# Optimization experiments

Hardware: AMD Instinct MI355X
Metric: run time of the kernel (lower is better)

The kernel has to match this reference:

```python
import jax, jax.numpy as jnp
import numpy as np

N, E = 50000, 500000
T, R, H, DK = 3, 5, 8, 16
IN = OUT = 128
SQRT_DK = float(np.sqrt(DK))
LN_EPS = 1e-5


def setup_inputs() -> dict:
    key = jax.random.key(0)
    ks = jax.random.split(key, 20)
    s = 0.05
    return {
        "x": jax.random.normal(ks[0], (N, IN), jnp.float32),
        "node_type": jax.random.randint(ks[1], (N,), 0, T),
        "src": jax.random.randint(ks[2], (E,), 0, N),
        "dst": jax.random.randint(ks[3], (E,), 0, N),
        "etype": jax.random.randint(ks[4], (E,), 0, R),
        "Wk": jax.random.normal(ks[5], (T, IN, OUT), jnp.float32) * s,
        "bk": jnp.zeros((T, OUT), jnp.float32),
        "Wq": jax.random.normal(ks[6], (T, IN, OUT), jnp.float32) * s,
        "bq": jnp.zeros((T, OUT), jnp.float32),
        "Wv": jax.random.normal(ks[7], (T, IN, OUT), jnp.float32) * s,
        "bv": jnp.zeros((T, OUT), jnp.float32),
        "Wa": jax.random.normal(ks[8], (T, OUT, OUT), jnp.float32) * s,
        "ba": jnp.zeros((T, OUT), jnp.float32),
        "rel_pri": jnp.ones((R, H), jnp.float32),
        "rel_att": jax.random.normal(ks[9], (R, H, DK, DK), jnp.float32) * s,
        "rel_msg": jax.random.normal(ks[10], (R, H, DK, DK), jnp.float32) * s,
        "skip": jnp.ones((T,), jnp.float32),
        "ln_g": jnp.ones((T, OUT), jnp.float32),
        "ln_b": jnp.zeros((T, OUT), jnp.float32),
    }


def _typed_proj(x, node_type, W, b):
    # apply all per-ntype Linears, then pick each node's own type
    y = jnp.einsum('ni,tio->nto', x, W) + b[None]            # [N,T,OUT]
    return jnp.take_along_axis(y, node_type[:, None, None], axis=1)[:, 0]


def reference(x, node_type, src, dst, etype, Wk, bk, Wq, bq, Wv, bv, Wa, ba,
              rel_pri, rel_att, rel_msg, skip, ln_g, ln_b):
    n = x.shape[0]
    k = _typed_proj(x, node_type, Wk, bk).reshape(n, H, DK)
    q = _typed_proj(x, node_type, Wq, bq).reshape(n, H, DK)
    v = _typed_proj(x, node_type, Wv, bv).reshape(n, H, DK)

    ks_e, vs_e, q_e = k[src], v[src], q[dst]                 # [E,H,DK]
    # relation-specific bmm: loop over the small fixed set of etypes
    key_e = jnp.zeros_like(ks_e)
    val_e = jnp.zeros_like(vs_e)
    for r in range(R):
        sel = (etype == r)[:, None, None].astype(x.dtype)
        key_e = key_e + sel * jnp.einsum('ehd,hdf->ehf', ks_e, rel_att[r])
        val_e = val_e + sel * jnp.einsum('ehd,hdf->ehf', vs_e, rel_msg[r])

    a = (q_e * key_e).sum(-1) * rel_pri[etype] / SQRT_DK     # [E,H]

    # segment softmax: per-(dst, etype) mailbox, matching DGL per-etype reduce
    seg = dst * R + etype
    NR = n * R
    m = jax.ops.segment_max(a, seg, num_segments=NR)         # [NR,H]
    m = jnp.where(jnp.isfinite(m), m, 0.0)
    p = jnp.exp(a - m[seg])
    denom = jax.ops.segment_sum(p, seg, num_segments=NR)
    attw = p / denom[seg]                                    # [E,H]

    h_seg = jax.ops.segment_sum(attw[..., None] * val_e, seg,
                                num_segments=NR).reshape(n, R, H, DK)
    cnt = jax.ops.segment_sum(jnp.ones((a.shape[0],), x.dtype), seg,
                              num_segments=NR).reshape(n, R)
    has = (cnt > 0).astype(x.dtype)                          # etypes with messages
    # cross_reducer='mean': average over etypes that delivered messages
    t = (h_seg * has[..., None, None]).sum(1)
    t = t / jnp.maximum(has.sum(1), 1.0)[:, None, None]
    t = t.reshape(n, OUT)

    trans = _typed_proj(t, node_type, Wa, ba)
    alpha = jax.nn.sigmoid(skip)[node_type][:, None]
    out = trans * alpha + x * (1.0 - alpha)

    # per-ntype LayerNorm (dropout is identity in eval)
    mu = out.mean(-1, keepdims=True)
    var = ((out - mu) ** 2).mean(-1, keepdims=True)
    out = (out - mu) * jax.lax.rsqrt(var + LN_EPS)
    out = out * ln_g[node_type] + ln_b[node_type]
    return out
```

## Files before the change

kernel.cpp:

```cpp
#include <hip/hip_runtime.h>
#include <math.h>

#define N_NODES 50000
#define N_EDGES 500000
#define NT 3
#define NRR 5
#define NH 8
#define DKH 16
#define DIM 128
#define NSEG (N_NODES * NRR)

__global__ void init_ints(int* __restrict__ base, long n_ints) {
  long i = (long)blockIdx.x * blockDim.x + threadIdx.x;
  long stride = (long)gridDim.x * blockDim.x;
  for (long j = i; j < n_ints; j += stride) base[j] = 0;
}

__global__ void bucket_nodes(const int* __restrict__ ntype, int* __restrict__ order,
                             int* __restrict__ bcnt) {
  __shared__ int lcnt[NT];
  __shared__ int lbase[NT];
  int tid = threadIdx.x;
  if (tid < NT) lcnt[tid] = 0;
  __syncthreads();
  int i = blockIdx.x * blockDim.x + tid;
  int t = -1, lp = 0;
  if (i < N_NODES) {
    t = ntype[i];
    lp = atomicAdd(&lcnt[t], 1);
  }
  __syncthreads();
  if (tid < NT) lbase[tid] = atomicAdd(&bcnt[tid], lcnt[tid]);
  __syncthreads();
  if (i < N_NODES) order[t * N_NODES + lbase[t] + lp] = i;
}

__global__ void hist_seg(const int* __restrict__ dst, const int* __restrict__ etype,
                         int* __restrict__ deg) {
  int i = blockIdx.x * blockDim.x + threadIdx.x;
  if (i >= N_EDGES) return;
  atomicAdd(&deg[dst[i] * NRR + etype[i]], 1);
}

__global__ void assign_seg(const int* __restrict__ deg, int* __restrict__ segstart,
                           int* __restrict__ gcursor) {
  int i = blockIdx.x * 256 + threadIdx.x;
  int lane = threadIdx.x & 63, wv = threadIdx.x >> 6;
  int d = (i < NSEG) ? deg[i] : 0;
  int s = d;
  #pragma unroll
  for (int m = 1; m < 64; m <<= 1) {
    int v = __shfl_up(s, m, 64);
    if (lane >= m) s += v;
  }
  __shared__ int wsum[4];
  __shared__ int wbase[4];
  __shared__ int blockbase;
  if (lane == 63) wsum[wv] = s;
  __syncthreads();
  if (threadIdx.x == 0) {
    int acc = 0;
    #pragma unroll
    for (int w = 0; w < 4; w++) { wbase[w] = acc; acc += wsum[w]; }
    blockbase = atomicAdd(gcursor, acc);
  }
  __syncthreads();
  if (i < NSEG) segstart[i] = blockbase + wbase[wv] + (s - d);
}

__global__ void scatter_seg(const int* __restrict__ src, const int* __restrict__ dst,
                            const int* __restrict__ etype,
                            const int* __restrict__ segstart, int* __restrict__ cursor,
                            int* __restrict__ meta) {
  int i = blockIdx.x * blockDim.x + threadIdx.x;
  if (i >= N_EDGES) return;
  int seg = dst[i] * NRR + etype[i];
  int pos = segstart[seg] + atomicAdd(&cursor[seg], 1);
  meta[pos] = src[i];
}

template<bool FUSED>
__launch_bounds__(256)
__global__ void typed_gemm(const float* __restrict__ in, const float* __restrict__ W,
                           const float* __restrict__ bias, float* __restrict__ out,
                           const int* __restrict__ order, const int* __restrict__ bcnt,
                           const float* __restrict__ hseg, const float* __restrict__ denom) {
  int t = blockIdx.y;
  int cnt = bcnt[t];
  int base = blockIdx.x * 64;
  if (base >= cnt) return;

  __shared__ float xs[64][129];
  __shared__ __align__(16) float wsl[16 * 128];
  __shared__ int nids[64];

  int tid = threadIdx.x;
  if (tid < 64) {
    int idx = base + tid;
    nids[tid] = (idx < cnt) ? order[t * N_NODES + idx] : -1;
  }
  __syncthreads();

  #pragma unroll
  for (int i = 0; i < 8; i++) {
    int idx = tid + i * 256;
    int node = idx >> 5;
    int c4 = idx & 31;
    int nid = nids[node];
    float4 v = make_float4(0.f, 0.f, 0.f, 0.f);
    if (nid >= 0) {
      if (FUSED) {
        int h = c4 >> 2;
        float cn = 0.f;
        float4 a = make_float4(0.f, 0.f, 0.f, 0.f);
        #pragma unroll
        for (int rr = 0; rr < NRR; rr++) {
          float den = denom[((size_t)nid * NRR + rr) * NH + h];
          if (den > 0.f) {
            float4 hv = *(const float4*)(hseg + ((size_t)nid * NRR + rr) * DIM + c4 * 4);
            a.x += hv.x; a.y += hv.y; a.z += hv.z; a.w += hv.w;
            cn += 1.f;
          }
        }
        float s = 1.f / fmaxf(cn, 1.f);
        v = make_float4(a.x * s, a.y * s, a.z * s, a.w * s);
      } else {
        v = *(const float4*)(in + (size_t)nid * DIM + c4 * 4);
      }
    }
    xs[node][c4 * 4 + 0] = v.x;
    xs[node][c4 * 4 + 1] = v.y;
    xs[node][c4 * 4 + 2] = v.z;
    xs[node][c4 * 4 + 3] = v.w;
  }

  const float* wbase = W + (size_t)t * DIM * DIM;
  int tx = tid & 15;
  int ty = tid >> 4;
  float4 acc[4][2];
  #pragma unroll
  for (int j = 0; j < 4; j++) {
    acc[j][0] = make_float4(0.f, 0.f, 0.f, 0.f);
    acc[j][1] = make_float4(0.f, 0.f, 0.f, 0.f);
  }

  for (int ks = 0; ks < 8; ks++) {
    __syncthreads();
    {
      const float4* g = (const float4*)(wbase + ks * 2048 + tid * 8);
      float4 w0 = g[0], w1 = g[1];
      *(float4*)&wsl[tid * 8] = w0;
      *(float4*)&wsl[tid * 8 + 4] = w1;
    }
    __syncthreads();
    #pragma unroll
    for (int kk = 0; kk < 16; kk++) {
      float4 w0 = *(const float4*)&wsl[kk * 128 + tx * 8];
      float4 w1 = *(const float4*)&wsl[kk * 128 + tx * 8 + 4];
      #pragma unroll
      for (int j = 0; j < 4; j++) {
        float xv = xs[ty * 4 + j][ks * 16 + kk];
        acc[j][0].x += xv * w0.x; acc[j][0].y += xv * w0.y;
        acc[j][0].z += xv * w0.z; acc[j][0].w += xv * w0.w;
        acc[j][1].x += xv * w1.x; acc[j][1].y += xv * w1.y;
        acc[j][1].z += xv * w1.z; acc[j][1].w += xv * w1.w;
      }
    }
  }

  float4 b0 = *(const float4*)(bias + t * DIM + tx * 8);
  float4 b1 = *(const float4*)(bias + t * DIM + tx * 8 + 4);
  #pragma unroll
  for (int j = 0; j < 4; j++) {
    int nid = nids[ty * 4 + j];
    if (nid < 0) continue;
    float4 o0 = make_float4(acc[j][0].x + b0.x, acc[j][0].y + b0.y,
                            acc[j][0].z + b0.z, acc[j][0].w + b0.w);
    float4 o1 = make_float4(acc[j][1].x + b1.x, acc[j][1].y + b1.y,
                            acc[j][1].z + b1.z, acc[j][1].w + b1.w);
    *(float4*)(out + (size_t)nid * DIM + tx * 8) = o0;
    *(float4*)(out + (size_t)nid * DIM + tx * 8 + 4) = o1;
  }
}

__launch_bounds__(256)
__global__ void rel_gather(const float* __restrict__ kmat, const float* __restrict__ qmat,
                           const float* __restrict__ vmat,
                           const float* __restrict__ rel_att, const float* __restrict__ rel_msg,
                           const float* __restrict__ rel_pri,
                           const int* __restrict__ segstart, const int* __restrict__ deg,
                           const int* __restrict__ meta,
                           float* __restrict__ denom, float* __restrict__ hseg) {
  int r = blockIdx.y;
  int tid = threadIdx.x;

  __shared__ __align__(16) float As[8 * 260];
  __shared__ __align__(16) float Ms[8 * 260];
  {
    int idx = tid * 8;
    int hh = idx >> 8, w = idx & 255;
    const float4* ga = (const float4*)(rel_att + (size_t)r * 2048 + idx);
    *(float4*)&As[hh * 260 + w] = ga[0];
    *(float4*)&As[hh * 260 + w + 4] = ga[1];
    const float4* gm = (const float4*)(rel_msg + (size_t)r * 2048 + idx);
    *(float4*)&Ms[hh * 260 + w] = gm[0];
    *(float4*)&Ms[hh * 260 + w + 4] = gm[1];
  }
  __syncthreads();

  int g = tid >> 3;
  int c = tid & 7;
  int n = blockIdx.x * 32 + g;
  if (n >= N_NODES) return;
  int seg = n * NRR + r;
  int dg = deg[seg];
  if (dg == 0) {
    denom[(size_t)seg * NH + c] = 0.f;
    return;
  }
  int p0 = segstart[seg];
  float pri = rel_pri[r * NH + c] * 0.25f;

  const float4* qr = (const float4*)(qmat + (size_t)n * DIM + c * DKH);
  float4 q0 = qr[0], q1 = qr[1], q2 = qr[2], q3 = qr[3];

  float qa[16];
  #pragma unroll
  for (int d = 0; d < 16; d++) {
    const float* ar = &As[c * 260 + d * 16];
    float4 a0 = *(const float4*)(ar);
    float4 a1 = *(const float4*)(ar + 4);
    float4 a2 = *(const float4*)(ar + 8);
    float4 a3 = *(const float4*)(ar + 12);
    qa[d] = a0.x*q0.x + a0.y*q0.y + a0.z*q0.z + a0.w*q0.w
          + a1.x*q1.x + a1.y*q1.y + a1.z*q1.z + a1.w*q1.w
          + a2.x*q2.x + a2.y*q2.y + a2.z*q2.z + a2.w*q2.w
          + a3.x*q3.x + a3.y*q3.y + a3.z*q3.z + a3.w*q3.w;
  }

  float den = 0.f;
  float pv[16];
  #pragma unroll
  for (int d = 0; d < 16; d++) pv[d] = 0.f;

  for (int e = 0; e < dg; e++) {
    int sn = meta[p0 + e];
    const float4* kr = (const float4*)(kmat + (size_t)sn * DIM + c * DKH);
    float4 k0 = kr[0], k1 = kr[1], k2 = kr[2], k3 = kr[3];
    const float4* vr = (const float4*)(vmat + (size_t)sn * DIM + c * DKH);
    float4 v0 = vr[0], v1 = vr[1], v2 = vr[2], v3 = vr[3];
    float s = k0.x*qa[0]  + k0.y*qa[1]  + k0.z*qa[2]  + k0.w*qa[3]
            + k1.x*qa[4]  + k1.y*qa[5]  + k1.z*qa[6]  + k1.w*qa[7]
            + k2.x*qa[8]  + k2.y*qa[9]  + k2.z*qa[10] + k2.w*qa[11]
            + k3.x*qa[12] + k3.y*qa[13] + k3.z*qa[14] + k3.w*qa[15];
    float p = __expf(s * pri);
    den += p;
    pv[0]  += p*v0.x; pv[1]  += p*v0.y; pv[2]  += p*v0.z; pv[3]  += p*v0.w;
    pv[4]  += p*v1.x; pv[5]  += p*v1.y; pv[6]  += p*v1.z; pv[7]  += p*v1.w;
    pv[8]  += p*v2.x; pv[9]  += p*v2.y; pv[10] += p*v2.z; pv[11] += p*v2.w;
    pv[12] += p*v3.x; pv[13] += p*v3.y; pv[14] += p*v3.z; pv[15] += p*v3.w;
  }

  float o[16];
  #pragma unroll
  for (int j = 0; j < 16; j++) o[j] = 0.f;
  #pragma unroll
  for (int d = 0; d < 16; d++) {
    const float* mr = &Ms[c * 260 + d * 16];
    float4 m0 = *(const float4*)(mr);
    float4 m1 = *(const float4*)(mr + 4);
    float4 m2 = *(const float4*)(mr + 8);
    float4 m3 = *(const float4*)(mr + 12);
    float p = pv[d];
    o[0]  += p*m0.x; o[1]  += p*m0.y; o[2]  += p*m0.z; o[3]  += p*m0.w;
    o[4]  += p*m1.x; o[5]  += p*m1.y; o[6]  += p*m1.z; o[7]  += p*m1.w;
    o[8]  += p*m2.x; o[9]  += p*m2.y; o[10] += p*m2.z; o[11] += p*m2.w;
    o[12] += p*m3.x; o[13] += p*m3.y; o[14] += p*m3.z; o[15] += p*m3.w;
  }
  float inv = 1.f / den;
  float4* hw = (float4*)(hseg + (size_t)seg * DIM + c * DKH);
  hw[0] = make_float4(o[0]*inv,  o[1]*inv,  o[2]*inv,  o[3]*inv);
  hw[1] = make_float4(o[4]*inv,  o[5]*inv,  o[6]*inv,  o[7]*inv);
  hw[2] = make_float4(o[8]*inv,  o[9]*inv,  o[10]*inv, o[11]*inv);
  hw[3] = make_float4(o[12]*inv, o[13]*inv, o[14]*inv, o[15]*inv);
  denom[(size_t)seg * NH + c] = den;
}

__launch_bounds__(256)
__global__ void blend_ln(const float* __restrict__ trans, const float* __restrict__ x,
                         const int* __restrict__ ntype, const float* __restrict__ skip,
                         const float* __restrict__ ln_g, const float* __restrict__ ln_b,
                         float* __restrict__ out) {
  int n = blockIdx.x * 4 + (threadIdx.x >> 6);
  int lane = threadIdx.x & 63;
  if (n >= N_NODES) return;
  int t = ntype[n];
  float alpha = 1.f / (1.f + __expf(-skip[t]));
  float beta = 1.f - alpha;
  size_t bo = (size_t)n * DIM;
  float o0 = trans[bo + lane] * alpha + x[bo + lane] * beta;
  float o1 = trans[bo + lane + 64] * alpha + x[bo + lane + 64] * beta;
  float s = o0 + o1;
  #pragma unroll
  for (int m = 32; m >= 1; m >>= 1) s += __shfl_xor(s, m, 64);
  float mu = s * (1.f / 128.f);
  float d0 = o0 - mu, d1 = o1 - mu;
  float sq = d0 * d0 + d1 * d1;
  #pragma unroll
  for (int m = 32; m >= 1; m >>= 1) sq += __shfl_xor(sq, m, 64);
  float rs = rsqrtf(sq * (1.f / 128.f) + 1e-5f);
  out[bo + lane]      = d0 * rs * ln_g[t * DIM + lane]      + ln_b[t * DIM + lane];
  out[bo + lane + 64] = d1 * rs * ln_g[t * DIM + lane + 64] + ln_b[t * DIM + lane + 64];
}

extern "C" void kernel_launch(void* const* d_in, const int* in_sizes, int n_in,
                              void* d_out, int out_size, void* d_ws, size_t ws_size,
                              hipStream_t stream) {
  const float* x       = (const float*)d_in[0];
  const int*   ntype   = (const int*)  d_in[1];
  const int*   src     = (const int*)  d_in[2];
  const int*   dst     = (const int*)  d_in[3];
  const int*   etype   = (const int*)  d_in[4];
  const float* Wk      = (const float*)d_in[5];
  const float* bk      = (const float*)d_in[6];
  const float* Wq      = (const float*)d_in[7];
  const float* bq      = (const float*)d_in[8];
  const float* Wv      = (const float*)d_in[9];
  const float* bv      = (const float*)d_in[10];
  const float* Wa      = (const float*)d_in[11];
  const float* ba      = (const float*)d_in[12];
  const float* rel_pri = (const float*)d_in[13];
  const float* rel_att = (const float*)d_in[14];
  const float* rel_msg = (const float*)d_in[15];
  const float* skip    = (const float*)d_in[16];
  const float* ln_g    = (const float*)d_in[17];
  const float* ln_b    = (const float*)d_in[18];
  float* out = (float*)d_out;

  float* ws = (float*)d_ws;
  size_t o = 0;
  float* kbuf = ws + o; o += (size_t)N_NODES * DIM;
  float* qbuf = ws + o; o += (size_t)N_NODES * DIM;
  float* vbuf = ws + o; o += (size_t)N_NODES * DIM;
  float* hseg  = ws + o; o += (size_t)NSEG * DIM;
  float* denom = ws + o; o += (size_t)NSEG * NH;
  int* order    = (int*)(ws + o); o += (size_t)N_NODES * NT;
  int* meta     = (int*)(ws + o); o += (size_t)N_EDGES;
  int* segstart = (int*)(ws + o); o += (size_t)NSEG;
  int* deg     = (int*)(ws + o); o += (size_t)NSEG;
  int* cursor  = (int*)(ws + o); o += (size_t)NSEG;
  int* cnts    = (int*)(ws + o); o += 8;
  (void)ws_size; (void)in_sizes; (void)n_in; (void)out_size;

  long nzero_ints = (long)NSEG * 2 + 8;
  init_ints<<<512, 256, 0, stream>>>(deg, nzero_ints);

  bucket_nodes<<<(N_NODES + 255) / 256, 256, 0, stream>>>(ntype, order, cnts);
  hist_seg<<<(N_EDGES + 255) / 256, 256, 0, stream>>>(dst, etype, deg);
  assign_seg<<<(NSEG + 255) / 256, 256, 0, stream>>>(deg, segstart, cnts + 4);
  scatter_seg<<<(N_EDGES + 255) / 256, 256, 0, stream>>>(src, dst, etype, segstart,
                                                         cursor, meta);

  dim3 gg((N_NODES + 63) / 64, NT);
  typed_gemm<false><<<gg, 256, 0, stream>>>(x, Wk, bk, kbuf, order, cnts, nullptr, nullptr);
  typed_gemm<false><<<gg, 256, 0, stream>>>(x, Wq, bq, qbuf, order, cnts, nullptr, nullptr);
  typed_gemm<false><<<gg, 256, 0, stream>>>(x, Wv, bv, vbuf, order, cnts, nullptr, nullptr);

  dim3 gr((N_NODES + 31) / 32, NRR);
  rel_gather<<<gr, 256, 0, stream>>>(kbuf, qbuf, vbuf, rel_att, rel_msg, rel_pri,
                                     segstart, deg, meta, denom, hseg);

  typed_gemm<true><<<gg, 256, 0, stream>>>(x, Wa, ba, qbuf, order, cnts, hseg, denom);

  blend_ln<<<(N_NODES + 3) / 4, 256, 0, stream>>>(qbuf, x, ntype, skip, ln_g, ln_b, out);
}
```

Measured before the change: 508.0 us.

## Fuse K/Q/V projections, interleave K/V rows, unroll gather, fuse LayerNorm into Wa GEMM

The three K/Q/V projection launches are merged into one kernel that stages each x tile in shared memory once and reuses it for all three weight matrices. K and V are written interleaved into one 256-wide row so each gathered source node reads contiguous memory. The per-edge loop in rel_gather is unrolled by two so more loads are in flight. The skip blend and LayerNorm are folded into the Wa GEMM epilogue, which removes the blend_ln launch and its round trip through global memory. In exchange the fused GEMM runs its three passes serially inside each block.

Measured after the change: 474.0 us. -6.7%, faster.

```diff
diff --git a/kernel.cpp b/kernel.cpp
--- a/kernel.cpp
+++ b/kernel.cpp
@@ -79,12 +79,13 @@
   meta[pos] = src[i];
 }
 
-template<bool FUSED>
 __launch_bounds__(256)
-__global__ void typed_gemm(const float* __restrict__ in, const float* __restrict__ W,
-                           const float* __restrict__ bias, float* __restrict__ out,
-                           const int* __restrict__ order, const int* __restrict__ bcnt,
-                           const float* __restrict__ hseg, const float* __restrict__ denom) {
+__global__ void kqv_gemm(const float* __restrict__ x,
+                         const float* __restrict__ Wk, const float* __restrict__ bk,
+                         const float* __restrict__ Wq, const float* __restrict__ bq,
+                         const float* __restrict__ Wv, const float* __restrict__ bv,
+                         float* __restrict__ kv, float* __restrict__ qb,
+                         const int* __restrict__ order, const int* __restrict__ bcnt) {
   int t = blockIdx.y;
   int cnt = bcnt[t];
   int base = blockIdx.x * 64;
@@ -104,37 +105,248 @@
   #pragma unroll
   for (int i = 0; i < 8; i++) {
     int idx = tid + i * 256;
-    int node = idx >> 5;
-    int c4 = idx & 31;
+    int node = idx >> 5, c4 = idx & 31;
     int nid = nids[node];
     float4 v = make_float4(0.f, 0.f, 0.f, 0.f);
-    if (nid >= 0) {
-      if (FUSED) {
-        int h = c4 >> 2;
-        float cn = 0.f;
-        float4 a = make_float4(0.f, 0.f, 0.f, 0.f);
-        #pragma unroll
-        for (int rr = 0; rr < NRR; rr++) {
-          float den = denom[((size_t)nid * NRR + rr) * NH + h];
-          if (den > 0.f) {
-            float4 hv = *(const float4*)(hseg + ((size_t)nid * NRR + rr) * DIM + c4 * 4);
-            a.x += hv.x; a.y += hv.y; a.z += hv.z; a.w += hv.w;
-            cn += 1.f;
-          }
-        }
-        float s = 1.f / fmaxf(cn, 1.f);
-        v = make_float4(a.x * s, a.y * s, a.z * s, a.w * s);
-      } else {
-        v = *(const float4*)(in + (size_t)nid * DIM + c4 * 4);
-      }
-    }
+    if (nid >= 0) v = *(const float4*)(x + (size_t)nid * DIM + c4 * 4);
     xs[node][c4 * 4 + 0] = v.x;
     xs[node][c4 * 4 + 1] = v.y;
     xs[node][c4 * 4 + 2] = v.z;
     xs[node][c4 * 4 + 3] = v.w;
   }
 
-  const float* wbase = W + (size_t)t * DIM * DIM;
+  int tx = tid & 15;
+  int ty = tid >> 4;
+  const float* Ws[3] = {Wk, Wv, Wq};
+  const float* bs[3] = {bk, bv, bq};
+
+  for (int m = 0; m < 3; m++) {
+    const float* wbase = Ws[m] + (size_t)t * DIM * DIM;
+    float4 acc[4][2];
+    #pragma unroll
+    for (int j = 0; j < 4; j++) {
+      acc[j][0] = make_float4(0.f, 0.f, 0.f, 0.f);
+      acc[j][1] = make_float4(0.f, 0.f, 0.f, 0.f);
+    }
+
+    for (int ks = 0; ks < 8; ks++) {
+      __syncthreads();
+      {
+        const float4* g = (const float4*)(wbase + ks * 2048 + tid * 8);
+        float4 w0 = g[0], w1 = g[1];
+        *(float4*)&wsl[tid * 8] = w0;
+        *(float4*)&wsl[tid * 8 + 4] = w1;
+      }
+      __syncthreads();
+      #pragma unroll
+      for (int kk = 0; kk < 16; kk++) {
+        float4 w0 = *(const float4*)&wsl[kk * 128 + tx * 8];
+        float4 w1 = *(const float4*)&wsl[kk * 128 + tx * 8 + 4];
+        #pragma unroll
+        for (int j = 0; j < 4; j++) {
+          float xv = xs[ty * 4 + j][ks * 16 + kk];
+          acc[j][0].x += xv * w0.x; acc[j][0].y += xv * w0.y;
+          acc[j][0].z += xv * w0.z; acc[j][0].w += xv * w0.w;
+          acc[j][1].x += xv * w1.x; acc[j][1].y += xv * w1.y;
+          acc[j][1].z += xv * w1.z; acc[j][1].w += xv * w1.w;
+        }
+      }
+    }
+
+    float4 b0 = *(const float4*)(bs[m] + t * DIM + tx * 8);
+    float4 b1 = *(const float4*)(bs[m] + t * DIM + tx * 8 + 4);
+    #pragma unroll
+    for (int j = 0; j < 4; j++) {
+      int nid = nids[ty * 4 + j];
+      if (nid < 0) continue;
+      float* ob = (m == 2) ? (qb + (size_t)nid * DIM)
+                           : (kv + (size_t)nid * 256 + (m == 1 ? 128 : 0));
+      *(float4*)(ob + tx * 8)     = make_float4(acc[j][0].x + b0.x, acc[j][0].y + b0.y,
+                                                acc[j][0].z + b0.z, acc[j][0].w + b0.w);
+      *(float4*)(ob + tx * 8 + 4) = make_float4(acc[j][1].x + b1.x, acc[j][1].y + b1.y,
+                                                acc[j][1].z + b1.z, acc[j][1].w + b1.w);
+    }
+  }
+}
+
+__launch_bounds__(256)
+__global__ void rel_gather(const float* __restrict__ kv, const float* __restrict__ qmat,
+                           const float* __restrict__ rel_att, const float* __restrict__ rel_msg,
+                           const float* __restrict__ rel_pri,
+                           const int* __restrict__ segstart, const int* __restrict__ deg,
+                           const int* __restrict__ meta,
+                           float* __restrict__ denom, float* __restrict__ hseg) {
+  int r = blockIdx.y;
+  int tid = threadIdx.x;
+
+  __shared__ __align__(16) float As[8 * 260];
+  __shared__ __align__(16) float Ms[8 * 260];
+  {
+    int idx = tid * 8;
+    int hh = idx >> 8, w = idx & 255;
+    const float4* ga = (const float4*)(rel_att + (size_t)r * 2048 + idx);
+    *(float4*)&As[hh * 260 + w] = ga[0];
+    *(float4*)&As[hh * 260 + w + 4] = ga[1];
+    const float4* gm = (const float4*)(rel_msg + (size_t)r * 2048 + idx);
+    *(float4*)&Ms[hh * 260 + w] = gm[0];
+    *(float4*)&Ms[hh * 260 + w + 4] = gm[1];
+  }
+  __syncthreads();
+
+  int g = tid >> 3;
+  int c = tid & 7;
+  int n = blockIdx.x * 32 + g;
+  if (n >= N_NODES) return;
+  int seg = n * NRR + r;
+  int dg = deg[seg];
+  if (dg == 0) {
+    denom[(size_t)seg * NH + c] = 0.f;
+    return;
+  }
+  int p0 = segstart[seg];
+  float pri = rel_pri[r * NH + c] * 0.25f;
+
+  const float4* qr = (const float4*)(qmat + (size_t)n * DIM + c * DKH);
+  float4 q0 = qr[0], q1 = qr[1], q2 = qr[2], q3 = qr[3];
+
+  float qa[16];
+  #pragma unroll
+  for (int d = 0; d < 16; d++) {
+    const float* ar = &As[c * 260 + d * 16];
+    float4 a0 = *(const float4*)(ar);
+    float4 a1 = *(const float4*)(ar + 4);
+    float4 a2 = *(const float4*)(ar + 8);
+    float4 a3 = *(const float4*)(ar + 12);
+    qa[d] = a0.x*q0.x + a0.y*q0.y + a0.z*q0.z + a0.w*q0.w
+          + a1.x*q1.x + a1.y*q1.y + a1.z*q1.z + a1.w*q1.w
+          + a2.x*q2.x + a2.y*q2.y + a2.z*q2.z + a2.w*q2.w
+          + a3.x*q3.x + a3.y*q3.y + a3.z*q3.z + a3.w*q3.w;
+  }
+
+  float den = 0.f;
+  float pv[16];
+  #pragma unroll
+  for (int d = 0; d < 16; d++) pv[d] = 0.f;
+
+#define SCORE(k0_, k1_, k2_, k3_) \
+  (k0_.x*qa[0]  + k0_.y*qa[1]  + k0_.z*qa[2]  + k0_.w*qa[3]  \
+ + k1_.x*qa[4]  + k1_.y*qa[5]  + k1_.z*qa[6]  + k1_.w*qa[7]  \
+ + k2_.x*qa[8]  + k2_.y*qa[9]  + k2_.z*qa[10] + k2_.w*qa[11] \
+ + k3_.x*qa[12] + k3_.y*qa[13] + k3_.z*qa[14] + k3_.w*qa[15])
+
+#define PVADD(p_, v0_, v1_, v2_, v3_) \
+  pv[0]  += p_*v0_.x; pv[1]  += p_*v0_.y; pv[2]  += p_*v0_.z; pv[3]  += p_*v0_.w; \
+  pv[4]  += p_*v1_.x; pv[5]  += p_*v1_.y; pv[6]  += p_*v1_.z; pv[7]  += p_*v1_.w; \
+  pv[8]  += p_*v2_.x; pv[9]  += p_*v2_.y; pv[10] += p_*v2_.z; pv[11] += p_*v2_.w; \
+  pv[12] += p_*v3_.x; pv[13] += p_*v3_.y; pv[14] += p_*v3_.z; pv[15] += p_*v3_.w;
+
+  int e = 0;
+  for (; e + 2 <= dg; e += 2) {
+    int sn0 = meta[p0 + e], sn1 = meta[p0 + e + 1];
+    const float4* r0 = (const float4*)(kv + (size_t)sn0 * 256 + c * DKH);
+    const float4* r1 = (const float4*)(kv + (size_t)sn1 * 256 + c * DKH);
+    float4 ka0 = r0[0], kb0 = r0[1], kc0 = r0[2], kd0 = r0[3];
+    float4 va0 = r0[32], vb0 = r0[33], vc0 = r0[34], vd0 = r0[35];
+    float4 ka1 = r1[0], kb1 = r1[1], kc1 = r1[2], kd1 = r1[3];
+    float4 va1 = r1[32], vb1 = r1[33], vc1 = r1[34], vd1 = r1[35];
+    float s0 = SCORE(ka0, kb0, kc0, kd0);
+    float s1 = SCORE(ka1, kb1, kc1, kd1);
+    float p0e = __expf(s0 * pri);
+    float p1e = __expf(s1 * pri);
+    den += p0e + p1e;
+    PVADD(p0e, va0, vb0, vc0, vd0);
+    PVADD(p1e, va1, vb1, vc1, vd1);
+  }
+  if (e < dg) {
+    int sn0 = meta[p0 + e];
+    const float4* r0 = (const float4*)(kv + (size_t)sn0 * 256 + c * DKH);
+    float4 ka0 = r0[0], kb0 = r0[1], kc0 = r0[2], kd0 = r0[3];
+    float4 va0 = r0[32], vb0 = r0[33], vc0 = r0[34], vd0 = r0[35];
+    float s0 = SCORE(ka0, kb0, kc0, kd0);
+    float p0e = __expf(s0 * pri);
+    den += p0e;
+    PVADD(p0e, va0, vb0, vc0, vd0);
+  }
+#undef SCORE
+#undef PVADD
+
+  float o[16];
+  #pragma unroll
+  for (int j = 0; j < 16; j++) o[j] = 0.f;
+  #pragma unroll
+  for (int d = 0; d < 16; d++) {
+    const float* mr = &Ms[c * 260 + d * 16];
+    float4 m0 = *(const float4*)(mr);
+    float4 m1 = *(const float4*)(mr + 4);
+    float4 m2 = *(const float4*)(mr + 8);
+    float4 m3 = *(const float4*)(mr + 12);
+    float p = pv[d];
+    o[0]  += p*m0.x; o[1]  += p*m0.y; o[2]  += p*m0.z; o[3]  += p*m0.w;
+    o[4]  += p*m1.x; o[5]  += p*m1.y; o[6]  += p*m1.z; o[7]  += p*m1.w;
+    o[8]  += p*m2.x; o[9]  += p*m2.y; o[10] += p*m2.z; o[11] += p*m2.w;
+    o[12] += p*m3.x; o[13] += p*m3.y; o[14] += p*m3.z; o[15] += p*m3.w;
+  }
+  float inv = 1.f / den;
+  float4* hw = (float4*)(hseg + (size_t)seg * DIM + c * DKH);
+  hw[0] = make_float4(o[0]*inv,  o[1]*inv,  o[2]*inv,  o[3]*inv);
+  hw[1] = make_float4(o[4]*inv,  o[5]*inv,  o[6]*inv,  o[7]*inv);
+  hw[2] = make_float4(o[8]*inv,  o[9]*inv,  o[10]*inv, o[11]*inv);
+  hw[3] = make_float4(o[12]*inv, o[13]*inv, o[14]*inv, o[15]*inv);
+  denom[(size_t)seg * NH + c] = den;
+}
+
+__launch_bounds__(256)
+__global__ void wa_gemm_ln(const float* __restrict__ hseg, const float* __restrict__ denom,
+                           const float* __restrict__ Wa, const float* __restrict__ ba,
+                           const float* __restrict__ x, const float* __restrict__ skip,
+                           const float* __restrict__ ln_g, const float* __restrict__ ln_b,
+                           float* __restrict__ out,
+                           const int* __restrict__ order, const int* __restrict__ bcnt) {
+  int t = blockIdx.y;
+  int cnt = bcnt[t];
+  int base = blockIdx.x * 64;
+  if (base >= cnt) return;
+
+  __shared__ float xs[64][129];
+  __shared__ __align__(16) float wsl[16 * 128];
+  __shared__ int nids[64];
+
+  int tid = threadIdx.x;
+  if (tid < 64) {
+    int idx = base + tid;
+    nids[tid] = (idx < cnt) ? order[t * N_NODES + idx] : -1;
+  }
+  __syncthreads();
+
+  #pragma unroll
+  for (int i = 0; i < 8; i++) {
+    int idx = tid + i * 256;
+    int node = idx >> 5, c4 = idx & 31;
+    int nid = nids[node];
+    float4 v = make_float4(0.f, 0.f, 0.f, 0.f);
+    if (nid >= 0) {
+      int h = c4 >> 2;
+      float cn = 0.f;
+      float4 a = make_float4(0.f, 0.f, 0.f, 0.f);
+      #pragma unroll
+      for (int rr = 0; rr < NRR; rr++) {
+        float den = denom[((size_t)nid * NRR + rr) * NH + h];
+        if (den > 0.f) {
+          float4 hv = *(const float4*)(hseg + ((size_t)nid * NRR + rr) * DIM + c4 * 4);
+          a.x += hv.x; a.y += hv.y; a.z += hv.z; a.w += hv.w;
+          cn += 1.f;
+        }
+      }
+      float s = 1.f / fmaxf(cn, 1.f);
+      v = make_float4(a.x * s, a.y * s, a.z * s, a.w * s);
+    }
+    xs[node][c4 * 4 + 0] = v.x;
+    xs[node][c4 * 4 + 1] = v.y;
+    xs[node][c4 * 4 + 2] = v.z;
+    xs[node][c4 * 4 + 3] = v.w;
+  }
+
+  const float* wbase = Wa + (size_t)t * DIM * DIM;
   int tx = tid & 15;
   int ty = tid >> 4;
   float4 acc[4][2];
@@ -168,149 +380,46 @@
     }
   }
 
-  float4 b0 = *(const float4*)(bias + t * DIM + tx * 8);
-  float4 b1 = *(const float4*)(bias + t * DIM + tx * 8 + 4);
+  float alpha = 1.f / (1.f + __expf(-skip[t]));
+  float beta = 1.f - alpha;
+  float4 b0 = *(const float4*)(ba + t * DIM + tx * 8);
+  float4 b1 = *(const float4*)(ba + t * DIM + tx * 8 + 4);
+  float4 g0 = *(const float4*)(ln_g + t * DIM + tx * 8);
+  float4 g1 = *(const float4*)(ln_g + t * DIM + tx * 8 + 4);
+  float4 e0 = *(const float4*)(ln_b + t * DIM + tx * 8);
+  float4 e1 = *(const float4*)(ln_b + t * DIM + tx * 8 + 4);
+
   #pragma unroll
   for (int j = 0; j < 4; j++) {
     int nid = nids[ty * 4 + j];
     if (nid < 0) continue;
-    float4 o0 = make_float4(acc[j][0].x + b0.x, acc[j][0].y + b0.y,
-                            acc[j][0].z + b0.z, acc[j][0].w + b0.w);
-    float4 o1 = make_float4(acc[j][1].x + b1.x, acc[j][1].y + b1.y,
-                            acc[j][1].z + b1.z, acc[j][1].w + b1.w);
-    *(float4*)(out + (size_t)nid * DIM + tx * 8) = o0;
-    *(float4*)(out + (size_t)nid * DIM + tx * 8 + 4) = o1;
-  }
-}
-
-__launch_bounds__(256)
-__global__ void rel_gather(const float* __restrict__ kmat, const float* __restrict__ qmat,
-                           const float* __restrict__ vmat,
-                           const float* __restrict__ rel_att, const float* __restrict__ rel_msg,
-                           const float* __restrict__ rel_pri,
-                           const int* __restrict__ segstart, const int* __restrict__ deg,
-                           const int* __restrict__ meta,
-                           float* __restrict__ denom, float* __restrict__ hseg) {
-  int r = blockIdx.y;
-  int tid = threadIdx.x;
-
-  __shared__ __align__(16) float As[8 * 260];
-  __shared__ __align__(16) float Ms[8 * 260];
-  {
-    int idx = tid * 8;
-    int hh = idx >> 8, w = idx & 255;
-    const float4* ga = (const float4*)(rel_att + (size_t)r * 2048 + idx);
-    *(float4*)&As[hh * 260 + w] = ga[0];
-    *(float4*)&As[hh * 260 + w + 4] = ga[1];
-    const float4* gm = (const float4*)(rel_msg + (size_t)r * 2048 + idx);
-    *(float4*)&Ms[hh * 260 + w] = gm[0];
-    *(float4*)&Ms[hh * 260 + w + 4] = gm[1];
-  }
-  __syncthreads();
-
-  int g = tid >> 3;
-  int c = tid & 7;
-  int n = blockIdx.x * 32 + g;
-  if (n >= N_NODES) return;
-  int seg = n * NRR + r;
-  int dg = deg[seg];
-  if (dg == 0) {
-    denom[(size_t)seg * NH + c] = 0.f;
-    return;
-  }
-  int p0 = segstart[seg];
-  float pri = rel_pri[r * NH + c] * 0.25f;
-
-  const float4* qr = (const float4*)(qmat + (size_t)n * DIM + c * DKH);
-  float4 q0 = qr[0], q1 = qr[1], q2 = qr[2], q3 = qr[3];
-
-  float qa[16];
-  #pragma unroll
-  for (int d = 0; d < 16; d++) {
-    const float* ar = &As[c * 260 + d * 16];
-    float4 a0 = *(const float4*)(ar);
-    float4 a1 = *(const float4*)(ar + 4);
-    float4 a2 = *(const float4*)(ar + 8);
-    float4 a3 = *(const float4*)(ar + 12);
-    qa[d] = a0.x*q0.x + a0.y*q0.y + a0.z*q0.z + a0.w*q0.w
-          + a1.x*q1.x + a1.y*q1.y + a1.z*q1.z + a1.w*q1.w
-          + a2.x*q2.x + a2.y*q2.y + a2.z*q2.z + a2.w*q2.w
-          + a3.x*q3.x + a3.y*q3.y + a3.z*q3.z + a3.w*q3.w;
-  }
-
-  float den = 0.f;
-  float pv[16];
-  #pragma unroll
-  for (int d = 0; d < 16; d++) pv[d] = 0.f;
-
-  for (int e = 0; e < dg; e++) {
-    int sn = meta[p0 + e];
-    const float4* kr = (const float4*)(kmat + (size_t)sn * DIM + c * DKH);
-    float4 k0 = kr[0], k1 = kr[1], k2 = kr[2], k3 = kr[3];
-    const float4* vr = (const float4*)(vmat + (size_t)sn * DIM + c * DKH);
-    float4 v0 = vr[0], v1 = vr[1], v2 = vr[2], v3 = vr[3];
-    float s = k0.x*qa[0]  + k0.y*qa[1]  + k0.z*qa[2]  + k0.w*qa[3]
-            + k1.x*qa[4]  + k1.y*qa[5]  + k1.z*qa[6]  + k1.w*qa[7]
-            + k2.x*qa[8]  + k2.y*qa[9]  + k2.z*qa[10] + k2.w*qa[11]
-            + k3.x*qa[12] + k3.y*qa[13] + k3.z*qa[14] + k3.w*qa[15];
-    float p = __expf(s * pri);
-    den += p;
-    pv[0]  += p*v0.x; pv[1]  += p*v0.y; pv[2]  += p*v0.z; pv[3]  += p*v0.w;
-    pv[4]  += p*v1.x; pv[5]  += p*v1.y; pv[6]  += p*v1.z; pv[7]  += p*v1.w;
-    pv[8]  += p*v2.x; pv[9]  += p*v2.y; pv[10] += p*v2.z; pv[11] += p*v2.w;
-    pv[12] += p*v3.x; pv[13] += p*v3.y; pv[14] += p*v3.z; pv[15] += p*v3.w;
-  }
-
-  float o[16];
-  #pragma unroll
-  for (int j = 0; j < 16; j++) o[j] = 0.f;
-  #pragma unroll
-  for (int d = 0; d < 16; d++) {
-    const float* mr = &Ms[c * 260 + d * 16];
-    float4 m0 = *(const float4*)(mr);
-    float4 m1 = *(const float4*)(mr + 4);
-    float4 m2 = *(const float4*)(mr + 8);
-    float4 m3 = *(const float4*)(mr + 12);
-    float p = pv[d];
-    o[0]  += p*m0.x; o[1]  += p*m0.y; o[2]  += p*m0.z; o[3]  += p*m0.w;
-    o[4]  += p*m1.x; o[5]  += p*m1.y; o[6]  += p*m1.z; o[7]  += p*m1.w;
-    o[8]  += p*m2.x; o[9]  += p*m2.y; o[10] += p*m2.z; o[11] += p*m2.w;
-    o[12] += p*m3.x; o[13] += p*m3.y; o[14] += p*m3.z; o[15] += p*m3.w;
-  }
-  float inv = 1.f / den;
-  float4* hw = (float4*)(hseg + (size_t)seg * DIM + c * DKH);
-  hw[0] = make_float4(o[0]*inv,  o[1]*inv,  o[2]*inv,  o[3]*inv);
-  hw[1] = make_float4(o[4]*inv,  o[5]*inv,  o[6]*inv,  o[7]*inv);
-  hw[2] = make_float4(o[8]*inv,  o[9]*inv,  o[10]*inv, o[11]*inv);
-  hw[3] = make_float4(o[12]*inv, o[13]*inv, o[14]*inv, o[15]*inv);
-  denom[(size_t)seg * NH + c] = den;
-}
-
-__launch_bounds__(256)
-__global__ void blend_ln(const float* __restrict__ trans, const float* __restrict__ x,
-                         const int* __restrict__ ntype, const float* __restrict__ skip,
-                         const float* __restrict__ ln_g, const float* __restrict__ ln_b,
-                         float* __restrict__ out) {
-  int n = blockIdx.x * 4 + (threadIdx.x >> 6);
-  int lane = threadIdx.x & 63;
-  if (n >= N_NODES) return;
-  int t = ntype[n];
-  float alpha = 1.f / (1.f + __expf(-skip[t]));
-  float beta = 1.f - alpha;
-  size_t bo = (size_t)n * DIM;
-  float o0 = trans[bo + lane] * alpha + x[bo + lane] * beta;
-  float o1 = trans[bo + lane + 64] * alpha + x[bo + lane + 64] * beta;
-  float s = o0 + o1;
-  #pragma unroll
-  for (int m = 32; m >= 1; m >>= 1) s += __shfl_xor(s, m, 64);
-  float mu = s * (1.f / 128.f);
-  float d0 = o0 - mu, d1 = o1 - mu;
-  float sq = d0 * d0 + d1 * d1;
-  #pragma unroll
-  for (int m = 32; m >= 1; m >>= 1) sq += __shfl_xor(sq, m, 64);
-  float rs = rsqrtf(sq * (1.f / 128.f) + 1e-5f);
-  out[bo + lane]      = d0 * rs * ln_g[t * DIM + lane]      + ln_b[t * DIM + lane];
-  out[bo + lane + 64] = d1 * rs * ln_g[t * DIM + lane + 64] + ln_b[t * DIM + lane + 64];
+    float4 xa = *(const float4*)(x + (size_t)nid * DIM + tx * 8);
+    float4 xb = *(const float4*)(x + (size_t)nid * DIM + tx * 8 + 4);
+    float o[8];
+    o[0] = (acc[j][0].x + b0.x) * alpha + xa.x * beta;
+    o[1] = (acc[j][0].y + b0.y) * alpha + xa.y * beta;
+    o[2] = (acc[j][0].z + b0.z) * alpha + xa.z * beta;
+    o[3] = (acc[j][0].w + b0.w) * alpha + xa.w * beta;
+    o[4] = (acc[j][1].x + b1.x) * alpha + xb.x * beta;
+    o[5] = (acc[j][1].y + b1.y) * alpha + xb.y * beta;
+    o[6] = (acc[j][1].z + b1.z) * alpha + xb.z * beta;
+    o[7] = (acc[j][1].w + b1.w) * alpha + xb.w * beta;
+    float s = o[0]+o[1]+o[2]+o[3]+o[4]+o[5]+o[6]+o[7];
+    #pragma unroll
+    for (int m = 1; m <= 8; m <<= 1) s += __shfl_xor(s, m);
+    float mu = s * (1.f / 128.f);
+    float sq = 0.f;
+    #pragma unroll
+    for (int i = 0; i < 8; i++) { o[i] -= mu; sq += o[i] * o[i]; }
+    #pragma unroll
+    for (int m = 1; m <= 8; m <<= 1) sq += __shfl_xor(sq, m);
+    float rs = rsqrtf(sq * (1.f / 128.f) + 1e-5f);
+    float* ob = out + (size_t)nid * DIM + tx * 8;
+    *(float4*)(ob)     = make_float4(o[0]*rs*g0.x + e0.x, o[1]*rs*g0.y + e0.y,
+                                     o[2]*rs*g0.z + e0.z, o[3]*rs*g0.w + e0.w);
+    *(float4*)(ob + 4) = make_float4(o[4]*rs*g1.x + e1.x, o[5]*rs*g1.y + e1.y,
+                                     o[6]*rs*g1.z + e1.z, o[7]*rs*g1.w + e1.w);
+  }
 }
 
 extern "C" void kernel_launch(void* const* d_in, const int* in_sizes, int n_in,
@@ -339,9 +448,8 @@
 
   float* ws = (float*)d_ws;
   size_t o = 0;
-  float* kbuf = ws + o; o += (size_t)N_NODES * DIM;
-  float* qbuf = ws + o; o += (size_t)N_NODES * DIM;
-  float* vbuf = ws + o; o += (size_t)N_NODES * DIM;
+  float* kvbuf = ws + o; o += (size_t)N_NODES * 256;
+  float* qbuf  = ws + o; o += (size_t)N_NODES * DIM;
   float* hseg  = ws + o; o += (size_t)NSEG * DIM;
   float* denom = ws + o; o += (size_t)NSEG * NH;
   int* order    = (int*)(ws + o); o += (size_t)N_NODES * NT;
@@ -362,15 +470,12 @@
                                                          cursor, meta);
 
   dim3 gg((N_NODES + 63) / 64, NT);
-  typed_gemm<false><<<gg, 256, 0, stream>>>(x, Wk, bk, kbuf, order, cnts, nullptr, nullptr);
-  typed_gemm<false><<<gg, 256, 0, stream>>>(x, Wq, bq, qbuf, order, cnts, nullptr, nullptr);
-  typed_gemm<false><<<gg, 256, 0, stream>>>(x, Wv, bv, vbuf, order, cnts, nullptr, nullptr);
+  kqv_gemm<<<gg, 256, 0, stream>>>(x, Wk, bk, Wq, bq, Wv, bv, kvbuf, qbuf, order, cnts);
 
   dim3 gr((N_NODES + 31) / 32, NRR);
-  rel_gather<<<gr, 256, 0, stream>>>(kbuf, qbuf, vbuf, rel_att, rel_msg, rel_pri,
+  rel_gather<<<gr, 256, 0, stream>>>(kvbuf, qbuf, rel_att, rel_msg, rel_pri,
                                      segstart, deg, meta, denom, hseg);
 
-  typed_gemm<true><<<gg, 256, 0, stream>>>(x, Wa, ba, qbuf, order, cnts, hseg, denom);
-
-  blend_ln<<<(N_NODES + 3) / 4, 256, 0, stream>>>(qbuf, x, ntype, skip, ln_g, ln_b, out);
-}
+  wa_gemm_ln<<<gg, 256, 0, stream>>>(hseg, denom, Wa, ba, x, skip, ln_g, ln_b, out,
+                                     order, cnts);
+}
```
